# Kernel optimization log

Hardware: AMD Instinct MI355X
Metric: run time of the kernel (lower is better)

Reference implementation:

```python
import jax, jax.numpy as jnp
import numpy as np

N_QUBITS = 8
N_CYCLES = 4
N_LAYERS = 2  # log2(8) - 1
B = 65536

CNOT = jnp.array([[1, 0, 0, 0],
                  [0, 1, 0, 0],
                  [0, 0, 0, 1],
                  [0, 0, 1, 0]], dtype=jnp.complex64)


def apply_gate(state, U, wires):
    """Apply a (2^k x 2^k) gate U on the given wires of state (B, 2,2,...,2).
    Wire 0 is the leftmost (most significant) qubit axis."""
    k = len(wires)
    src = [w + 1 for w in wires]
    dst = list(range(1, 1 + k))
    st = jnp.moveaxis(state, src, dst)
    shp = st.shape
    st = st.reshape(shp[0], 2 ** k, -1)
    st = jnp.einsum('ij,bjr->bir', U, st)
    return jnp.moveaxis(st.reshape(shp), dst, src)


def apply_ry(state, q, angles):
    """Batched RY(angle) on qubit q; angles has shape (B,)."""
    st = jnp.moveaxis(state, q + 1, 1)  # (B, 2, rest...)
    c = jnp.cos(0.5 * angles).reshape((-1,) + (1,) * (st.ndim - 2))
    s = jnp.sin(0.5 * angles).reshape((-1,) + (1,) * (st.ndim - 2))
    s0, s1 = st[:, 0], st[:, 1]
    new = jnp.stack([c * s0 - s * s1, s * s0 + c * s1], axis=1)
    return jnp.moveaxis(new, 1, q + 1)


def crx_mat(theta):
    c = (jnp.cos(0.5 * theta) + 0j).astype(jnp.complex64)
    s = (-1j * jnp.sin(0.5 * theta)).astype(jnp.complex64)
    one = jnp.ones((), jnp.complex64)
    zero = jnp.zeros((), jnp.complex64)
    return jnp.stack([
        jnp.stack([one, zero, zero, zero]),
        jnp.stack([zero, one, zero, zero]),
        jnp.stack([zero, zero, c, s]),
        jnp.stack([zero, zero, s, c]),
    ])


def u3_mat(p):
    th, ph, lm = p[0], p[1], p[2]
    ct = (jnp.cos(0.5 * th) + 0j).astype(jnp.complex64)
    st = (jnp.sin(0.5 * th) + 0j).astype(jnp.complex64)
    el = jnp.exp(1j * lm).astype(jnp.complex64)
    ep = jnp.exp(1j * ph).astype(jnp.complex64)
    return jnp.stack([
        jnp.stack([ct, -el * st]),
        jnp.stack([ep * st, ep * el * ct]),
    ])


def expval_z(state, q):
    st = jnp.moveaxis(state, q + 1, 1)
    p = (st.real ** 2 + st.imag ** 2).reshape(st.shape[0], 2, -1).sum(-1)
    return p[:, 0] - p[:, 1]


def _forward(x, crx_theta, u3_params, w1, b1, w2, b2):
    b = x.shape[0]
    # |0...0> initial state, shape (B, 2,2,...,2)
    state = jnp.zeros((b, 2 ** N_QUBITS), jnp.complex64).at[:, 0].set(1.0)
    state = state.reshape((b,) + (2,) * N_QUBITS)
    # encoder: data re-uploading RY angle encoding + CNOT ring, n_cycles times
    for _ in range(N_CYCLES):
        for q in range(N_QUBITS):
            state = apply_ry(state, q, x[:, q])
        for q in range(N_QUBITS):
            state = apply_gate(state, CNOT, [q, (q + 1) % N_QUBITS])
    # QCNN conv/pool layers with shared weights per layer
    active = list(range(N_QUBITS))
    for layer in range(N_LAYERS):
        U = crx_mat(crx_theta[layer])
        for i in range(0, len(active) - 1, 2):
            state = apply_gate(state, U, [active[i], active[i + 1]])
        for i in range(1, len(active) - 1, 2):
            state = apply_gate(state, U, [active[i], active[i + 1]])
        remain = active[1::2]
        # mid-circuit expval in the original is discarded and does not alter state
        V = u3_mat(u3_params[layer])
        for q in remain:
            state = apply_gate(state, V, [q])
        active = remain
    feats = jnp.stack([expval_z(state, q) for q in active], axis=1)  # (B, 2)
    h = jnp.tanh(feats @ w1 + b1)
    return jax.nn.sigmoid(h @ w2 + b2)  # (B, 1)


def setup_inputs() -> dict:
    key = jax.random.key(0)
    ks = jax.random.split(key, 6)
    return {
        'x': jax.random.normal(ks[0], (B, N_QUBITS), jnp.float32),
        'crx_theta': jax.random.normal(ks[1], (N_LAYERS,), jnp.float32),
        'u3_params': jax.random.normal(ks[2], (N_LAYERS, 3), jnp.float32),
        'w1': jax.random.normal(ks[3], (2, 10), jnp.float32) * 0.5,
        'b1': jnp.zeros((10,), jnp.float32),
        'w2': jax.random.normal(ks[4], (10, 1), jnp.float32) * 0.5,
        'b2': jnp.zeros((1,), jnp.float32),
    }


def reference(x, crx_theta, u3_params, w1, b1, w2, b2):
    return _forward(x, crx_theta, u3_params, w1, b1, w2, b2)
```

## Files before the change

kernel.cpp:

```cpp
#include <hip/hip_runtime.h>


#define NQ 8
typedef _Float16 h2 __attribute__((ext_vector_type(2)));

__device__ __forceinline__ float h2f(h2 v){ return __builtin_bit_cast(float, v); }
__device__ __forceinline__ h2 f2h(float v){ return __builtin_bit_cast(h2, v); }
__device__ __forceinline__ h2 u2h(unsigned u){ return __builtin_bit_cast(h2, u); }
__device__ __forceinline__ h2 negh(h2 v){ return __builtin_bit_cast(h2, __builtin_bit_cast(unsigned, v) ^ 0x80008000u); }
__device__ __forceinline__ h2 mk(float x){ _Float16 h=(_Float16)x; return (h2){h,h}; }
__device__ __forceinline__ h2 mk2(float a, float b){ return (h2){(_Float16)a,(_Float16)b}; }
__device__ __forceinline__ h2 fma2h(h2 a, h2 b, h2 c){ return __builtin_elementwise_fma(a,b,c); }
__device__ __forceinline__ h2 swp(h2 v){ return __builtin_shufflevector(v,v,1,0); }

template<int CTRL>
__device__ __forceinline__ float dppf(float v){
    return __int_as_float(__builtin_amdgcn_mov_dpp(__float_as_int(v), CTRL, 0xF, 0xF, true));
}
template<int M>
__device__ __forceinline__ float sx(float v){
    if constexpr (M==1)       return dppf<0xB1>(v);
    else if constexpr (M==2)  return dppf<0x4E>(v);
    else if constexpr (M==32) return __shfl_xor(v, 32, 64);
    else return __int_as_float(__builtin_amdgcn_ds_swizzle(__float_as_int(v), (M<<10)|0x1F));
}
__device__ __forceinline__ float bperm(int ba, float v){
    return __int_as_float(__builtin_amdgcn_ds_bpermute(ba, __float_as_int(v)));
}
__device__ __forceinline__ void cmulh(h2&R, h2&I, h2 C, h2 S, h2 nS){
    h2 nR = fma2h(C, R, nS*I);
    I = fma2h(C, I, S*R);
    R = nR;
}

#define FOR_E _Pragma("unroll") for (int e = 0; e < 2; ++e)

__global__ void qcnn_prep(const float* __restrict__ crx,
                          const float* __restrict__ u3p,
                          unsigned* __restrict__ ws){
    if (threadIdx.x==0 && blockIdx.x==0){
        auto PK=[](float lo, float hi)->unsigned{
            unsigned a=__builtin_bit_cast(unsigned short,(_Float16)lo);
            unsigned b=__builtin_bit_cast(unsigned short,(_Float16)hi);
            return a | (b<<16);
        };
        float sc0,cc0,sc1,cc1;
        __sincosf(0.5f*crx[0],&sc0,&cc0);
        __sincosf(0.5f*crx[1],&sc1,&cc1);
        ws[0]=PK(cc0,cc0); ws[1]=PK(sc0,sc0); ws[2]=PK(cc1,cc1); ws[3]=PK(sc1,sc1);
        float th0=u3p[0], ph0=u3p[1], lm0=u3p[2];
        float ust0,uct0; __sincosf(0.5f*th0,&ust0,&uct0);
        ws[4]=PK(uct0,uct0); ws[5]=PK(ust0,ust0); ws[6]=PK(-ust0,-ust0); ws[7]=PK(-ust0,ust0);
        float th1=u3p[3], ph1=u3p[4], lm1=u3p[5];
        float ust1,uct1; __sincosf(0.5f*th1,&ust1,&uct1);
        float sl1,cl1;   __sincosf(lm1,&sl1,&cl1);
        float sp1,cp1;   __sincosf(ph1,&sp1,&cp1);
        ws[8]=PK(uct1,uct1); ws[9]=PK(ust1,ust1); ws[10]=PK(-ust1,-ust1);
        ws[11]=PK(cl1,cl1); ws[12]=PK(sl1,sl1); ws[13]=PK(cp1,cp1); ws[14]=PK(sp1,sp1);
        float cpl1=cp1*cl1-sp1*sl1, spl1=sp1*cl1+cp1*sl1;
        float u01r=-ust1*cl1, u01i=-ust1*sl1;
        float u10r= ust1*cp1, u10i= ust1*sp1;
        float u11r= uct1*cpl1, u11i= uct1*spl1;
        ws[15]=PK(uct1,u11r); ws[16]=PK(u01r,u10r); ws[17]=PK(0.f,-u11i);
        ws[18]=PK(-u01i,-u10i); ws[19]=PK(0.f,u11i); ws[20]=PK(u01i,u10i);
        for(int k=0;k<4;++k){
            float kf=(float)k, sA,cA,sB,cB,sA2,cA2,sB2,cB2;
            __sincosf(lm0*kf,      &sA,&cA);
            __sincosf(lm0*(kf+1.f),&sB,&cB);
            __sincosf(ph0*kf,      &sA2,&cA2);
            __sincosf(ph0*(kf+1.f),&sB2,&cB2);
            unsigned* q = ws + 24 + k*4;
            q[0]=PK(cA,cB); q[1]=PK(sA,sB); q[2]=PK(cA2,cB2); q[3]=PK(sA2,sB2);
        }
    }
}

__global__ __launch_bounds__(256) void qcnn_kernel(
    const float* __restrict__ x,
    const unsigned* __restrict__ wsu,
    const float* __restrict__ w1,
    const float* __restrict__ b1,
    const float* __restrict__ w2,
    const float* __restrict__ b2,
    float* __restrict__ out,
    int Btot)
{
    const int gtid = blockIdx.x*256 + threadIdx.x;
    const int wv = gtid >> 6;
    const int l = threadIdx.x & 63;
    const int e0 = wv * 2;
    if (e0 >= Btot) return;
    const bool L5=(l>>5)&1, L4=(l>>4)&1, L3=(l>>3)&1, L2=(l>>2)&1, L1=(l>>1)&1, L0=l&1;

    const bool pb = __builtin_popcount(l) & 1;
    const int ba0 = (((l&32)|((l^(l>>1))&31)) << 2);
    const int ba1 = ba0 ^ (48<<2);

    h2 cH[2][6], tsH[2][6];
    h2 c6h[2], s6h[2], ns6h[2], c7h[2], sv7h[2];
    h2 A[2], B[2];
    const bool bits[6]={L5,L4,L3,L2,L1,L0};
    FOR_E {
        const float4* xv = (const float4*)(x + (e0+e)*NQ);
        float4 xa=xv[0], xb=xv[1];
        float ang[8]={xa.x,xa.y,xa.z,xa.w,xb.x,xb.y,xb.z,xb.w};
        float cq[8], sq[8];
#pragma unroll
        for(int q=0;q<8;++q) __sincosf(0.5f*ang[q], &sq[q], &cq[q]);
#pragma unroll
        for(int q=0;q<6;++q){
            cH[e][q]=mk(cq[q]);
            h2 sh=mk(sq[q]);
            tsH[e][q]= bits[q] ? sh : negh(sh);
        }
        c6h[e]=mk(cq[6]); s6h[e]=mk(sq[6]); ns6h[e]=negh(s6h[e]);
        c7h[e]=mk(cq[7]); sv7h[e]=mk2(-sq[7], sq[7]);
        float pl = (L5?sq[0]:cq[0])*(L4?sq[1]:cq[1])*(L3?sq[2]:cq[2])
                 * (L2?sq[3]:cq[3])*(L1?sq[4]:cq[4])*(L0?sq[5]:cq[5]);
        float pc6=pl*cq[6], ps6=pl*sq[6];
        A[e] = mk2(pc6*cq[7], pc6*sq[7]);
        B[e] = mk2(ps6*cq[7], ps6*sq[7]);
    }

    const h2 cc0h=u2h(wsu[0]), sn0h=u2h(wsu[1]), cc1h=u2h(wsu[2]), sn1h=u2h(wsu[3]);
    const h2 nsn0h=negh(sn0h), nsn1h=negh(sn1h);
    const h2 uct0h=u2h(wsu[4]), ust0h=u2h(wsu[5]), nust0h=u2h(wsu[6]), usv0h=u2h(wsu[7]);
    const h2 uct1h=u2h(wsu[8]), ust1h=u2h(wsu[9]), nust1h=u2h(wsu[10]);
    const h2 cl1h=u2h(wsu[11]), sl1h=u2h(wsu[12]), nsl1h=negh(sl1h);
    const h2 cp1h=u2h(wsu[13]), sp1h=u2h(wsu[14]), nsp1h=negh(sp1h);
    const h2 E0h=u2h(wsu[15]), E1h=u2h(wsu[16]), E2h=u2h(wsu[17]);
    const h2 E3h=u2h(wsu[18]), G2h=u2h(wsu[19]), G3h=u2h(wsu[20]);
    const int ki = (int)L4 + (int)L2 + (int)L0;
    uint4 dt = *(const uint4*)(wsu + 24 + ki*4);
    const h2 Clm=u2h(dt.x), Slm=u2h(dt.y), Cph=u2h(dt.z), Sph=u2h(dt.w);
    const h2 nSlm=negh(Slm), nSph=negh(Sph);
    const h2 tu1H = L4 ? ust0h : nust0h;
    const h2 tu3H = L2 ? ust0h : nust0h;
    const h2 tu5H = L0 ? ust0h : nust0h;

#define RY_L(q, M) do { FOR_E { \
    h2 oA = f2h(sx<M>(h2f(A[e]))), oB = f2h(sx<M>(h2f(B[e]))); \
    A[e] = fma2h(cH[e][q], A[e], tsH[e][q]*oA); \
    B[e] = fma2h(cH[e][q], B[e], tsH[e][q]*oB); } \
} while(0)

#define RINGF() do { FOR_E { \
    float TA = h2f(pb ? B[e] : A[e]); \
    float TS = h2f(swp(pb ? A[e] : B[e])); \
    float u0 = bperm(ba0, TA), u1 = bperm(ba1, TA); \
    float w0 = bperm(ba0, TS), w1 = bperm(ba1, TS); \
    A[e] = (h2){ f2h(u0).x, f2h(u1).y }; \
    B[e] = (h2){ f2h(w0).x, f2h(w1).y }; } \
} while(0)

    RINGF();
#pragma unroll
    for(int cyc=0;cyc<3;++cyc){
        RY_L(0,32); RY_L(1,16); RY_L(2,8); RY_L(3,4); RY_L(4,2); RY_L(5,1);
        FOR_E { h2 nA = fma2h(c6h[e], A[e], ns6h[e]*B[e]);
                h2 nB = fma2h(s6h[e], A[e], c6h[e]*B[e]);
                A[e]=nA; B[e]=nB; }
        FOR_E { A[e] = fma2h(c7h[e], A[e], sv7h[e]*swp(A[e]));
                B[e] = fma2h(c7h[e], B[e], sv7h[e]*swp(B[e])); }
        RINGF();
    }

    h2 RA[2], RB[2], IA[2], IB[2];
    FOR_E { RA[e]=A[e]; RB[e]=B[e]; IA[e]=(h2){0,0}; IB[e]=(h2){0,0}; }

#define SHF4(M) h2 oRA[2], oIA[2], oRB[2], oIB[2]; \
    FOR_E { oRA[e]=f2h(sx<M>(h2f(RA[e]))); oIA[e]=f2h(sx<M>(h2f(IA[e]))); \
            oRB[e]=f2h(sx<M>(h2f(RB[e]))); oIB[e]=f2h(sx<M>(h2f(IB[e]))); }
#define CRX_LL(CSH, M, cc, sn, nsn) do { \
    const bool ct = (l >> (CSH)) & 1; \
    SHF4(M) \
    if (ct) { FOR_E { \
        RA[e] = fma2h(cc, RA[e], (sn)*oIA[e]); IA[e] = fma2h(cc, IA[e], (nsn)*oRA[e]); \
        RB[e] = fma2h(cc, RB[e], (sn)*oIB[e]); IB[e] = fma2h(cc, IB[e], (nsn)*oRB[e]); } } \
} while(0)
#define RYC0(M, T) do { \
    SHF4(M) \
    FOR_E { \
    RA[e] = fma2h(uct0h, RA[e], (T)*oRA[e]); IA[e] = fma2h(uct0h, IA[e], (T)*oIA[e]); \
    RB[e] = fma2h(uct0h, RB[e], (T)*oRB[e]); IB[e] = fma2h(uct0h, IB[e], (T)*oIB[e]); } \
} while(0)

    {   h2 oA[2], oB[2];
        FOR_E { oA[e]=f2h(sx<16>(h2f(RA[e]))); oB[e]=f2h(sx<16>(h2f(RB[e]))); }
        if (L5){ FOR_E {
            IA[e] = nsn0h*oA[e]; RA[e] = cc0h*RA[e];
            IB[e] = nsn0h*oB[e]; RB[e] = cc0h*RB[e]; } }
    }
    CRX_LL(3, 4, cc0h, sn0h, nsn0h);
    CRX_LL(1, 1, cc0h, sn0h, nsn0h);
    FOR_E {
        h2 oI = swp(IB[e]), oR = swp(RB[e]);
        RB[e] = fma2h(cc0h, RB[e], sn0h*oI);
        IB[e] = fma2h(cc0h, IB[e], nsn0h*oR);
    }
    CRX_LL(4, 8, cc0h, sn0h, nsn0h);
    CRX_LL(2, 2, cc0h, sn0h, nsn0h);
    if (L0) { FOR_E {
        h2 nRA = fma2h(cc0h, RA[e], sn0h*IB[e]);
        h2 nRB = fma2h(cc0h, RB[e], sn0h*IA[e]);
        h2 nIA = fma2h(cc0h, IA[e], nsn0h*RB[e]);
        h2 nIB = fma2h(cc0h, IB[e], nsn0h*RA[e]);
        RA[e]=nRA; RB[e]=nRB; IA[e]=nIA; IB[e]=nIB; } }
    FOR_E { cmulh(RA[e],IA[e],Clm,Slm,nSlm); cmulh(RB[e],IB[e],Clm,Slm,nSlm); }
    RYC0(16, tu1H);
    RYC0(4,  tu3H);
    RYC0(1,  tu5H);
    FOR_E {
        h2 sA=swp(RA[e]), sB=swp(RB[e]), tA=swp(IA[e]), tB=swp(IB[e]);
        RA[e] = fma2h(uct0h, RA[e], usv0h*sA); RB[e] = fma2h(uct0h, RB[e], usv0h*sB);
        IA[e] = fma2h(uct0h, IA[e], usv0h*tA); IB[e] = fma2h(uct0h, IB[e], usv0h*tB);
    }
    FOR_E { cmulh(RA[e],IA[e],Cph,Sph,nSph); cmulh(RB[e],IB[e],Cph,Sph,nSph); }

    CRX_LL(4, 4, cc1h, sn1h, nsn1h);
    if (L0) { FOR_E {
        h2 sIA=swp(IA[e]), sRA=swp(RA[e]), sIB=swp(IB[e]), sRB=swp(RB[e]);
        RA[e] = fma2h(cc1h, RA[e], sn1h*sIA); IA[e] = fma2h(cc1h, IA[e], nsn1h*sRA);
        RB[e] = fma2h(cc1h, RB[e], sn1h*sIB); IB[e] = fma2h(cc1h, IB[e], nsn1h*sRB); } }
    CRX_LL(2, 1, cc1h, sn1h, nsn1h);
    {
        if (L2){ FOR_E { cmulh(RA[e],IA[e],cl1h,sl1h,nsl1h); cmulh(RB[e],IB[e],cl1h,sl1h,nsl1h); } }
        h2 T = L2 ? ust1h : nust1h;
        SHF4(4)
        FOR_E {
            RA[e] = fma2h(uct1h, RA[e], T*oRA[e]); IA[e] = fma2h(uct1h, IA[e], T*oIA[e]);
            RB[e] = fma2h(uct1h, RB[e], T*oRB[e]); IB[e] = fma2h(uct1h, IB[e], T*oIB[e]);
        }
        if (L2){ FOR_E { cmulh(RA[e],IA[e],cp1h,sp1h,nsp1h); cmulh(RB[e],IB[e],cp1h,sp1h,nsp1h); } }
    }
    FOR_E {
        h2 sR=swp(RA[e]), sI=swp(IA[e]);
        h2 nR = fma2h(E3h,sI, fma2h(E2h,IA[e], fma2h(E1h,sR, E0h*RA[e])));
        h2 nI = fma2h(G3h,sR, fma2h(G2h,RA[e], fma2h(E1h,sI, E0h*IA[e])));
        RA[e]=nR; IA[e]=nI;
        h2 sR2=swp(RB[e]), sI2=swp(IB[e]);
        h2 nR2 = fma2h(E3h,sI2, fma2h(E2h,IB[e], fma2h(E1h,sR2, E0h*RB[e])));
        h2 nI2 = fma2h(G3h,sR2, fma2h(G2h,RB[e], fma2h(E1h,sI2, E0h*IB[e])));
        RB[e]=nR2; IB[e]=nI2;
    }

    float f0[2], f1[2];
    FOR_E {
        float r0=(float)RA[e].x, r1=(float)RA[e].y, r2=(float)RB[e].x, r3=(float)RB[e].y;
        float i0=(float)IA[e].x, i1=(float)IA[e].y, i2=(float)IB[e].x, i3=(float)IB[e].y;
        float n0=fmaf(i0,i0,r0*r0), n1=fmaf(i1,i1,r1*r1);
        float n2=fmaf(i2,i2,r2*r2), n3=fmaf(i3,i3,r3*r3);
        float tot=(n0+n1)+(n2+n3);
        f0[e] = L2 ? -tot : tot;
        f1[e] = (n0-n1)+(n2-n3);
    }
    FOR_E { f0[e] += sx<1>(f0[e]);  f1[e] += sx<1>(f1[e]);  }
    FOR_E { f0[e] += sx<2>(f0[e]);  f1[e] += sx<2>(f1[e]);  }
    FOR_E { f0[e] += sx<4>(f0[e]);  f1[e] += sx<4>(f1[e]);  }
    FOR_E { f0[e] += sx<8>(f0[e]);  f1[e] += sx<8>(f1[e]);  }
    FOR_E { f0[e] += sx<16>(f0[e]); f1[e] += sx<16>(f1[e]); }
    FOR_E { f0[e] += sx<32>(f0[e]); f1[e] += sx<32>(f1[e]); }

    const int k = l & 15;
    const int row = l >> 4;
    const float Fx = (row & 1) ? f0[1] : f0[0];
    const float Fy = (row & 1) ? f1[1] : f1[0];
    float contrib = 0.0f;
    if (k < 10) {
        float z = fmaf(Fx, w1[k], fmaf(Fy, w1[10+k], b1[k]));
        float ex = __expf(2.0f*z);
        contrib = ((ex-1.0f)/(ex+1.0f)) * w2[k];
    }
    contrib += sx<1>(contrib);
    contrib += sx<2>(contrib);
    contrib += sx<4>(contrib);
    contrib += sx<8>(contrib);
    if (k == 0 && row < 2) {
        float a = contrib + b2[0];
        out[e0 + row] = 1.0f/(1.0f + __expf(-a));
    }
}

extern "C" void kernel_launch(void* const* d_in, const int* in_sizes, int n_in,
                              void* d_out, int out_size, void* d_ws, size_t ws_size,
                              hipStream_t stream) {
    const float* x   = (const float*)d_in[0];
    const float* crx = (const float*)d_in[1];
    const float* u3p = (const float*)d_in[2];
    const float* w1  = (const float*)d_in[3];
    const float* b1  = (const float*)d_in[4];
    const float* w2  = (const float*)d_in[5];
    const float* b2  = (const float*)d_in[6];
    float* out = (float*)d_out;
    unsigned* ws = (unsigned*)d_ws;

    const int B = in_sizes[0] / NQ;
    hipLaunchKernelGGL(qcnn_prep, dim3(1), dim3(64), 0, stream, crx, u3p, ws);
    const int waves = (B + 1) / 2;
    const int wavesPerBlock = 4;
    const int grid = (waves + wavesPerBlock - 1) / wavesPerBlock;
    hipLaunchKernelGGL(qcnn_kernel, dim3(grid), dim3(256), 0, stream,
                       x, ws, w1, b1, w2, b2, out, B);
}
```

Measured before the change: 118.5 us.

## Process four batch elements per wavefront with routed butterfly reduction

```diff
diff --git a/kernel.cpp b/kernel.cpp
--- a/kernel.cpp
+++ b/kernel.cpp
@@ -2,6 +2,7 @@
 
 
 #define NQ 8
+#define NE 4
 typedef _Float16 h2 __attribute__((ext_vector_type(2)));
 
 __device__ __forceinline__ float h2f(h2 v){ return __builtin_bit_cast(float, v); }
@@ -33,7 +34,7 @@
     R = nR;
 }
 
-#define FOR_E _Pragma("unroll") for (int e = 0; e < 2; ++e)
+#define FOR_E _Pragma("unroll") for (int e = 0; e < NE; ++e)
 
 __global__ void qcnn_prep(const float* __restrict__ crx,
                           const float* __restrict__ u3p,
@@ -88,7 +89,7 @@
     const int gtid = blockIdx.x*256 + threadIdx.x;
     const int wv = gtid >> 6;
     const int l = threadIdx.x & 63;
-    const int e0 = wv * 2;
+    const int e0 = wv * NE;
     if (e0 >= Btot) return;
     const bool L5=(l>>5)&1, L4=(l>>4)&1, L3=(l>>3)&1, L2=(l>>2)&1, L1=(l>>1)&1, L0=l&1;
 
@@ -96,12 +97,13 @@
     const int ba0 = (((l&32)|((l^(l>>1))&31)) << 2);
     const int ba1 = ba0 ^ (48<<2);
 
-    h2 cH[2][6], tsH[2][6];
-    h2 c6h[2], s6h[2], ns6h[2], c7h[2], sv7h[2];
-    h2 A[2], B[2];
+    h2 cH[NE][6], tsH[NE][6];
+    h2 c6h[NE], s6h[NE], ns6h[NE], c7h[NE], sv7h[NE];
+    h2 A[NE], B[NE];
     const bool bits[6]={L5,L4,L3,L2,L1,L0};
     FOR_E {
-        const float4* xv = (const float4*)(x + (e0+e)*NQ);
+        const int ee = (e0 + e < Btot) ? (e0 + e) : (Btot - 1);
+        const float4* xv = (const float4*)(x + ee*NQ);
         float4 xa=xv[0], xb=xv[1];
         float ang[8]={xa.x,xa.y,xa.z,xa.w,xb.x,xb.y,xb.z,xb.w};
         float cq[8], sq[8];
@@ -165,10 +167,10 @@
         RINGF();
     }
 
-    h2 RA[2], RB[2], IA[2], IB[2];
+    h2 RA[NE], RB[NE], IA[NE], IB[NE];
     FOR_E { RA[e]=A[e]; RB[e]=B[e]; IA[e]=(h2){0,0}; IB[e]=(h2){0,0}; }
 
-#define SHF4(M) h2 oRA[2], oIA[2], oRB[2], oIB[2]; \
+#define SHF4(M) h2 oRA[NE], oIA[NE], oRB[NE], oIB[NE]; \
     FOR_E { oRA[e]=f2h(sx<M>(h2f(RA[e]))); oIA[e]=f2h(sx<M>(h2f(IA[e]))); \
             oRB[e]=f2h(sx<M>(h2f(RB[e]))); oIB[e]=f2h(sx<M>(h2f(IB[e]))); }
 #define CRX_LL(CSH, M, cc, sn, nsn) do { \
@@ -185,7 +187,7 @@
     RB[e] = fma2h(uct0h, RB[e], (T)*oRB[e]); IB[e] = fma2h(uct0h, IB[e], (T)*oIB[e]); } \
 } while(0)
 
-    {   h2 oA[2], oB[2];
+    {   h2 oA[NE], oB[NE];
         FOR_E { oA[e]=f2h(sx<16>(h2f(RA[e]))); oB[e]=f2h(sx<16>(h2f(RB[e]))); }
         if (L5){ FOR_E {
             IA[e] = nsn0h*oA[e]; RA[e] = cc0h*RA[e];
@@ -244,7 +246,7 @@
         RB[e]=nR2; IB[e]=nI2;
     }
 
-    float f0[2], f1[2];
+    float f0[NE], f1[NE];
     FOR_E {
         float r0=(float)RA[e].x, r1=(float)RA[e].y, r2=(float)RB[e].x, r3=(float)RB[e].y;
         float i0=(float)IA[e].x, i1=(float)IA[e].y, i2=(float)IB[e].x, i3=(float)IB[e].y;
@@ -254,20 +256,30 @@
         f0[e] = L2 ? -tot : tot;
         f1[e] = (n0-n1)+(n2-n3);
     }
-    FOR_E { f0[e] += sx<1>(f0[e]);  f1[e] += sx<1>(f1[e]);  }
-    FOR_E { f0[e] += sx<2>(f0[e]);  f1[e] += sx<2>(f1[e]);  }
-    FOR_E { f0[e] += sx<4>(f0[e]);  f1[e] += sx<4>(f1[e]);  }
-    FOR_E { f0[e] += sx<8>(f0[e]);  f1[e] += sx<8>(f1[e]);  }
-    FOR_E { f0[e] += sx<16>(f0[e]); f1[e] += sx<16>(f1[e]); }
-    FOR_E { f0[e] += sx<32>(f0[e]); f1[e] += sx<32>(f1[e]); }
+
+#define ROUTED_REDUCE(F, OUTV) do { \
+    float u01 = L4 ? F[1] : F[0]; \
+    float w01 = L4 ? F[0] : F[1]; \
+    u01 += sx<16>(w01); \
+    float u23 = L4 ? F[3] : F[2]; \
+    float w23 = L4 ? F[2] : F[3]; \
+    u23 += sx<16>(w23); \
+    float v  = L5 ? u23 : u01; \
+    float w  = L5 ? u01 : u23; \
+    v += sx<32>(w); \
+    v += sx<8>(v); v += sx<4>(v); v += sx<2>(v); v += sx<1>(v); \
+    OUTV = v; \
+} while(0)
+
+    float F0, F1;
+    ROUTED_REDUCE(f0, F0);
+    ROUTED_REDUCE(f1, F1);
 
     const int k = l & 15;
     const int row = l >> 4;
-    const float Fx = (row & 1) ? f0[1] : f0[0];
-    const float Fy = (row & 1) ? f1[1] : f1[0];
     float contrib = 0.0f;
     if (k < 10) {
-        float z = fmaf(Fx, w1[k], fmaf(Fy, w1[10+k], b1[k]));
+        float z = fmaf(F0, w1[k], fmaf(F1, w1[10+k], b1[k]));
         float ex = __expf(2.0f*z);
         contrib = ((ex-1.0f)/(ex+1.0f)) * w2[k];
     }
@@ -275,7 +287,7 @@
     contrib += sx<2>(contrib);
     contrib += sx<4>(contrib);
     contrib += sx<8>(contrib);
-    if (k == 0 && row < 2) {
+    if (k == 0 && e0 + row < Btot) {
         float a = contrib + b2[0];
         out[e0 + row] = 1.0f/(1.0f + __expf(-a));
     }
@@ -296,7 +308,7 @@
 
     const int B = in_sizes[0] / NQ;
     hipLaunchKernelGGL(qcnn_prep, dim3(1), dim3(64), 0, stream, crx, u3p, ws);
-    const int waves = (B + 1) / 2;
+    const int waves = (B + NE - 1) / NE;
     const int wavesPerBlock = 4;
     const int grid = (waves + wavesPerBlock - 1) / wavesPerBlock;
     hipLaunchKernelGGL(qcnn_kernel, dim3(grid), dim3(256), 0, stream,
```

Measured after the change: 118.2 us. About the same (-0.3%).
